# Optimization experiments

Measured on AMD Instinct MI355X. Metric: run time of the kernel, lower is better.

Reference implementation:

```python
import jax, jax.numpy as jnp
import numpy as np

DIM = 1024
NUM_HEADS = 16
HEAD_DIM = DIM // NUM_HEADS
PHI = (1 + 5 ** 0.5) / 2


def setup_inputs() -> dict:
    key = jax.random.key(0)
    ks = jax.random.split(key, 9)
    s = 1.0 / np.sqrt(DIM)
    x = jax.random.normal(ks[0], (1, 4096, DIM), dtype=jnp.float32)
    Wq = jax.random.uniform(ks[1], (DIM, DIM), jnp.float32, -s, s)
    bq = jax.random.uniform(ks[2], (DIM,), jnp.float32, -s, s)
    Wk = jax.random.uniform(ks[3], (DIM, DIM), jnp.float32, -s, s)
    bk = jax.random.uniform(ks[4], (DIM,), jnp.float32, -s, s)
    Wv = jax.random.uniform(ks[5], (DIM, DIM), jnp.float32, -s, s)
    bv = jax.random.uniform(ks[6], (DIM,), jnp.float32, -s, s)
    Wo = jax.random.uniform(ks[7], (DIM, DIM), jnp.float32, -s, s)
    bo = jax.random.uniform(ks[8], (DIM,), jnp.float32, -s, s)
    return {"x": x, "Wq": Wq, "bq": bq, "Wk": Wk, "bk": bk,
            "Wv": Wv, "bv": bv, "Wo": Wo, "bo": bo}


def reference(x, Wq, bq, Wk, bk, Wv, bv, Wo, bo):
    B, S, _ = x.shape
    H, D = NUM_HEADS, HEAD_DIM
    scale = D ** (-0.5)
    # projections, reshape to [B, H, S, D]
    q = (x @ Wq.T + bq).reshape(B, S, H, D).transpose(0, 2, 1, 3)
    k = (x @ Wk.T + bk).reshape(B, S, H, D).transpose(0, 2, 1, 3)
    v = (x @ Wv.T + bv).reshape(B, S, H, D).transpose(0, 2, 1, 3)
    attn = jnp.einsum('bhqd,bhkd->bhqk', q, k) * scale
    attn = jax.nn.softmax(attn, axis=-1)
    # fractal per-head scalar modulation: phi^{-i} for head i
    scales = PHI ** (-jnp.arange(H, dtype=jnp.float32))
    attn = attn * scales[None, :, None, None]
    out = jnp.einsum('bhqk,bhkd->bhqd', attn, v)
    out = out.transpose(0, 2, 1, 3).reshape(B, S, H * D)
    return out @ Wo.T + bo
```

## Files before the change

kernel.cpp:

```cpp
#include <hip/hip_runtime.h>


typedef unsigned short u16;
typedef unsigned int u32;
typedef __attribute__((ext_vector_type(8))) short short8;
typedef __attribute__((ext_vector_type(4))) float f32x4;
typedef __attribute__((ext_vector_type(4))) u16 u16x4;
typedef __attribute__((ext_vector_type(4))) u32 u32x4;

#define KDIM 1024
#define QSCALE 0.18033688011112042f
#define LOG2PHI 0.6942419136306174f

__device__ __forceinline__ u16 f2bf(float f) {
  u32 u = __builtin_bit_cast(u32, f);
  u32 r = (u + 0x7fffu + ((u >> 16) & 1u)) >> 16;
  return (u16)r;
}

__device__ __forceinline__ u32 cvtpk(float lo, float hi) {
  u32 r;
  asm("v_cvt_pk_bf16_f32 %0, %1, %2" : "=v"(r) : "v"(lo), "v"(hi));
  return r;
}

#define EXP2(x) __builtin_amdgcn_exp2f(x)

__device__ __forceinline__ f32x4 fzero() {
  f32x4 z; z[0] = 0.f; z[1] = 0.f; z[2] = 0.f; z[3] = 0.f; return z;
}

__global__ __launch_bounds__(256) void cvt_kernel(const float* __restrict__ src,
                                                  u16* __restrict__ dst, int n4) {
  int i = blockIdx.x * 256 + threadIdx.x;
  if (i >= n4) return;
  f32x4 v = *(const f32x4*)(src + (size_t)i * 4);
  u16x4 o;
  o[0] = f2bf(v[0]); o[1] = f2bf(v[1]); o[2] = f2bf(v[2]); o[3] = f2bf(v[3]);
  *(u16x4*)(dst + (size_t)i * 4) = o;
}

template <int MODE>
__global__ __launch_bounds__(256) void gemm_bt(
    const u16* __restrict__ A, const u16* __restrict__ Bw,
    const float* __restrict__ bias0, const float* __restrict__ bias1,
    const float* __restrict__ bias2,
    u16* __restrict__ qo, u16* __restrict__ ko, u16* __restrict__ vto,
    float* __restrict__ co) {
  __shared__ u16 As[128 * 64];
  __shared__ u16 Bs[128 * 64];
  const int tid = threadIdx.x;
  const int w = tid >> 6, lane = tid & 63;
  const int wr = w >> 1, wc = w & 1;
  const int bm = blockIdx.x, bn = blockIdx.y;
  const int lr = lane & 15, lg = lane >> 4;
  const int srow8 = lane >> 3;
  const int schunk = lane & 7;

  f32x4 acc[4][4];
#pragma unroll
  for (int m = 0; m < 4; ++m)
#pragma unroll
    for (int n = 0; n < 4; ++n) acc[m][n] = fzero();

  for (int kt = 0; kt < KDIM / 64; ++kt) {
#pragma unroll
    for (int it = 0; it < 4; ++it) {
      const int rowt = (w * 4 + it) * 8 + srow8;
      const int ck = schunk ^ (rowt & 7);
      const u16* sa = A + (size_t)(bm * 128 + rowt) * KDIM + kt * 64 + ck * 8;
      const u16* sb = Bw + (size_t)(bn * 128 + rowt) * KDIM + kt * 64 + ck * 8;
      auto ga = (const __attribute__((address_space(1))) u32*)sa;
      auto la = (__attribute__((address_space(3))) u32*)&As[(w * 4 + it) * 512];
      __builtin_amdgcn_global_load_lds(ga, la, 16, 0, 0);
      auto gb = (const __attribute__((address_space(1))) u32*)sb;
      auto lb = (__attribute__((address_space(3))) u32*)&Bs[(w * 4 + it) * 512];
      __builtin_amdgcn_global_load_lds(gb, lb, 16, 0, 0);
    }
    __syncthreads();
#pragma unroll
    for (int kk = 0; kk < 2; ++kk) {
      short8 af[4], bf[4];
#pragma unroll
      for (int m = 0; m < 4; ++m) {
        const int row = wr * 64 + m * 16 + lr;
        const int kb = kk * 64 + lg * 16;
        af[m] = *(const short8*)((const char*)As + row * 128 + (kb ^ ((row & 7) << 4)));
      }
#pragma unroll
      for (int n = 0; n < 4; ++n) {
        const int row = wc * 64 + n * 16 + lr;
        const int kb = kk * 64 + lg * 16;
        bf[n] = *(const short8*)((const char*)Bs + row * 128 + (kb ^ ((row & 7) << 4)));
      }
#pragma unroll
      for (int m = 0; m < 4; ++m)
#pragma unroll
        for (int n = 0; n < 4; ++n)
          acc[m][n] = __builtin_amdgcn_mfma_f32_16x16x32_bf16(af[m], bf[n], acc[m][n], 0, 0, 0);
    }
    __syncthreads();
  }

#pragma unroll
  for (int m = 0; m < 4; ++m) {
#pragma unroll
    for (int n = 0; n < 4; ++n) {
#pragma unroll
      for (int r = 0; r < 4; ++r) {
        const int srow = bm * 128 + wr * 64 + m * 16 + lg * 4 + r;
        const int col = bn * 128 + wc * 64 + n * 16 + lr;
        float v = acc[m][n][r];
        if (MODE == 0) {
          const int which = col >> 10;
          const int hd = col & 1023;
          const int h = hd >> 6, d = hd & 63;
          const float* bp = (which == 0) ? bias0 : (which == 1) ? bias1 : bias2;
          v += bp[hd];
          if (which == 0) {
            qo[(size_t)h * 262144 + (size_t)srow * 64 + d] = f2bf(v * QSCALE);
          } else if (which == 1) {
            ko[(size_t)h * 262144 + (size_t)srow * 64 + d] = f2bf(v);
          } else {
            const int k5 = srow & 31;
            const int kap = ((k5 >> 2) & 3) * 8 + ((k5 >> 4) & 1) * 4 + (k5 & 3);
            vto[(size_t)h * 262144 + (size_t)d * 4096 + (srow & ~31) + kap] = f2bf(v);
          }
        } else {
          co[(size_t)srow * 1024 + col] = v + bias0[col];
        }
      }
    }
  }
}

__global__ __launch_bounds__(256) void attn_kernel(const u16* __restrict__ Q,
                                                   const u16* __restrict__ K,
                                                   const u16* __restrict__ VT,
                                                   u16* __restrict__ O) {
  __shared__ u16 Ks[2][2][4096];
  __shared__ u16 Vs[2][2][4096];
  const int tid = threadIdx.x;
  const int w = tid >> 6, lane = tid & 63;
  const int qsub = w >> 1, kh = w & 1;
  const int bid = blockIdx.x;
  const int id2 = (bid & 7) * 64 + (bid >> 3);
  const int h = id2 >> 5, qt = id2 & 31;
  const int lr = lane & 15, lg = lane >> 4;
  const int qrow0 = qt * 128 + qsub * 64;

  const u16* kg = K + (size_t)h * 262144;
  const u16* vg = VT + (size_t)h * 262144;

  short8 qf[4][2];
#pragma unroll
  for (int qg = 0; qg < 4; ++qg)
#pragma unroll
    for (int dg = 0; dg < 2; ++dg)
      qf[qg][dg] = *(const short8*)(Q + (size_t)h * 262144 +
                                    (size_t)(qrow0 + qg * 16 + lr) * 64 + dg * 32 + lg * 8);

#define STAGE1(KH, B, J)                                                      \
  do {                                                                        \
    _Pragma("unroll")                                                         \
    for (int it = 0; it < 2; ++it) {                                          \
      const int c = it * 256 + tid;                                           \
      const int row = c >> 3;                                                 \
      const int sc = (c & 7) ^ (row & 7);                                     \
      const u16* gk = kg + (size_t)((J) + row) * 64 + sc * 8;                 \
      __builtin_amdgcn_global_load_lds(                                       \
          (const __attribute__((address_space(1))) u32*)gk,                   \
          (__attribute__((address_space(3))) u32*)&Ks[KH][B][c * 8], 16, 0, 0); \
      const u16* gv = vg + (size_t)row * 4096 + (J) + sc * 8;                 \
      __builtin_amdgcn_global_load_lds(                                       \
          (const __attribute__((address_space(1))) u32*)gv,                   \
          (__attribute__((address_space(3))) u32*)&Vs[KH][B][c * 8], 16, 0, 0); \
    }                                                                         \
  } while (0)
#define STAGE(B, T) do { STAGE1(0, B, (T) * 64); STAGE1(1, B, 2048 + (T) * 64); } while (0)

  f32x4 o[4][4];
#pragma unroll
  for (int dg = 0; dg < 4; ++dg)
#pragma unroll
    for (int qg = 0; qg < 4; ++qg) o[dg][qg] = fzero();
  float lsum[4] = {0.f, 0.f, 0.f, 0.f};

  STAGE(0, 0);
  __syncthreads();

  int b = 0;
  for (int t = 0; t < 32; ++t) {
    if (t < 31) STAGE(b ^ 1, t + 1);
    u32x4 pb[2][4];
#pragma unroll
    for (int half = 0; half < 2; ++half) {
      f32x4 s[2][4];
#pragma unroll
      for (int ki = 0; ki < 2; ++ki) {
        const int row = (half * 2 + ki) * 16 + lr;
        const int sw = (row & 7) << 4;
        const char* base = (const char*)&Ks[kh][b][0] + row * 128;
        const short8 k0 = *(const short8*)(base + ((lg * 16) ^ sw));
        const short8 k1 = *(const short8*)(base + ((64 + lg * 16) ^ sw));
#pragma unroll
        for (int qg = 0; qg < 4; ++qg) {
          s[ki][qg] = __builtin_amdgcn_mfma_f32_16x16x32_bf16(k0, qf[qg][0], fzero(), 0, 0, 0);
          s[ki][qg] = __builtin_amdgcn_mfma_f32_16x16x32_bf16(k1, qf[qg][1], s[ki][qg], 0, 0, 0);
        }
      }
#pragma unroll
      for (int qg = 0; qg < 4; ++qg) {
        float rs = 0.f;
#pragma unroll
        for (int ki = 0; ki < 2; ++ki)
#pragma unroll
          for (int r = 0; r < 4; ++r) {
            const float e = EXP2(s[ki][qg][r]);
            s[ki][qg][r] = e;
            rs += e;
          }
        lsum[qg] += rs;
        pb[half][qg][0] = cvtpk(s[0][qg][0], s[0][qg][1]);
        pb[half][qg][1] = cvtpk(s[0][qg][2], s[0][qg][3]);
        pb[half][qg][2] = cvtpk(s[1][qg][0], s[1][qg][1]);
        pb[half][qg][3] = cvtpk(s[1][qg][2], s[1][qg][3]);
      }
    }
#pragma unroll
    for (int dg = 0; dg < 4; ++dg) {
      const int row = dg * 16 + lr;
      const int sw = (row & 7) << 4;
      const char* base = (const char*)&Vs[kh][b][0] + row * 128;
      const short8 v0 = *(const short8*)(base + ((lg * 16) ^ sw));
      const short8 v1 = *(const short8*)(base + ((64 + lg * 16) ^ sw));
#pragma unroll
      for (int qg = 0; qg < 4; ++qg) {
        o[dg][qg] = __builtin_amdgcn_mfma_f32_16x16x32_bf16(
            v0, __builtin_bit_cast(short8, pb[0][qg]), o[dg][qg], 0, 0, 0);
        o[dg][qg] = __builtin_amdgcn_mfma_f32_16x16x32_bf16(
            v1, __builtin_bit_cast(short8, pb[1][qg]), o[dg][qg], 0, 0, 0);
      }
    }
    __syncthreads();
    b ^= 1;
  }
#undef STAGE
#undef STAGE1

#pragma unroll
  for (int qg = 0; qg < 4; ++qg) {
    lsum[qg] += __shfl_xor(lsum[qg], 16, 64);
    lsum[qg] += __shfl_xor(lsum[qg], 32, 64);
  }

  float* cO = (float*)&Ks[0][0][0];
  float* cL = (float*)&Vs[0][0][0];
  if (kh == 1) {
#pragma unroll
    for (int qg = 0; qg < 4; ++qg) {
#pragma unroll
      for (int dg = 0; dg < 4; ++dg)
        *(f32x4*)(cO + qsub * 4096 + (qg * 4 + dg) * 256 + lane * 4) = o[dg][qg];
      cL[qsub * 64 + qg * 16 + lr] = lsum[qg];
    }
  }
  __syncthreads();
  if (kh == 0) {
    const float hs = EXP2(-(float)h * LOG2PHI);
#pragma unroll
    for (int qg = 0; qg < 4; ++qg) {
      const float l = fmaxf(lsum[qg] + cL[qsub * 64 + qg * 16 + lr], 1e-10f);
      const float sc = hs / l;
#pragma unroll
      for (int dg = 0; dg < 4; ++dg) {
        const f32x4 oth = *(const f32x4*)(cO + qsub * 4096 + (qg * 4 + dg) * 256 + lane * 4);
        u16x4 pk;
#pragma unroll
        for (int r = 0; r < 4; ++r) pk[r] = f2bf((o[dg][qg][r] + oth[r]) * sc);
        *(u16x4*)(O + (size_t)(qrow0 + qg * 16 + lr) * 1024 + h * 64 + dg * 16 + lg * 4) = pk;
      }
    }
  }
}

extern "C" void kernel_launch(void* const* d_in, const int* in_sizes, int n_in,
                              void* d_out, int out_size, void* d_ws, size_t ws_size,
                              hipStream_t stream) {
  const float* x = (const float*)d_in[0];
  const float* Wq = (const float*)d_in[1];
  const float* bq = (const float*)d_in[2];
  const float* Wk = (const float*)d_in[3];
  const float* bk = (const float*)d_in[4];
  const float* Wv = (const float*)d_in[5];
  const float* bv = (const float*)d_in[6];
  const float* Wo = (const float*)d_in[7];
  const float* bo = (const float*)d_in[8];
  float* out = (float*)d_out;

  u16* xb = (u16*)d_ws;
  u16* wqkv = xb + 4194304;
  u16* wob = wqkv + 3145728;
  u16* qs = wob + 1048576;
  u16* ks = qs + 4194304;
  u16* vt = ks + 4194304;
  u16* ob = xb;

  cvt_kernel<<<4096, 256, 0, stream>>>(x, xb, 1048576);
  cvt_kernel<<<1024, 256, 0, stream>>>(Wq, wqkv, 262144);
  cvt_kernel<<<1024, 256, 0, stream>>>(Wk, wqkv + 1048576, 262144);
  cvt_kernel<<<1024, 256, 0, stream>>>(Wv, wqkv + 2097152, 262144);
  cvt_kernel<<<1024, 256, 0, stream>>>(Wo, wob, 262144);

  gemm_bt<0><<<dim3(32, 24), 256, 0, stream>>>(xb, wqkv, bq, bk, bv, qs, ks, vt, nullptr);
  attn_kernel<<<512, 256, 0, stream>>>(qs, ks, vt, ob);
  gemm_bt<1><<<dim3(32, 8), 256, 0, stream>>>(ob, wob, bo, nullptr, nullptr,
                                              nullptr, nullptr, nullptr, out);
}
```

Baseline: 168.0 us.

## Store V in MFMA fragment order and load it directly to registers

The QKV projection now writes V in a layout where each lane's 8-element MFMA operand is contiguous. This lets the attention kernel load V fragments straight from global memory into registers instead of staging them through LDS, which frees half the shared memory and removes the V LDS traffic. The five weight and input conversion launches are also merged into one kernel. The trade-off is that V loads are issued synchronously each iteration without double buffering, so their latency may be exposed.

```diff
diff --git a/kernel.cpp b/kernel.cpp
--- a/kernel.cpp
+++ b/kernel.cpp
@@ -30,14 +30,24 @@
   f32x4 z; z[0] = 0.f; z[1] = 0.f; z[2] = 0.f; z[3] = 0.f; return z;
 }
 
-__global__ __launch_bounds__(256) void cvt_kernel(const float* __restrict__ src,
-                                                  u16* __restrict__ dst, int n4) {
-  int i = blockIdx.x * 256 + threadIdx.x;
-  if (i >= n4) return;
-  f32x4 v = *(const f32x4*)(src + (size_t)i * 4);
+__global__ __launch_bounds__(256) void cvt_all(
+    const float* __restrict__ x, const float* __restrict__ wq,
+    const float* __restrict__ wk, const float* __restrict__ wv,
+    const float* __restrict__ wo, u16* __restrict__ xb,
+    u16* __restrict__ wqkv, u16* __restrict__ wob) {
+  const int i = blockIdx.x * 256 + threadIdx.x;
+  const float* src;
+  u16* dst;
+  int off;
+  if (i < 1048576) { src = x; dst = xb; off = i; }
+  else if (i < 1310720) { src = wq; dst = wqkv; off = i - 1048576; }
+  else if (i < 1572864) { src = wk; dst = wqkv + 1048576; off = i - 1310720; }
+  else if (i < 1835008) { src = wv; dst = wqkv + 2097152; off = i - 1572864; }
+  else { src = wo; dst = wob; off = i - 1835008; }
+  f32x4 v = *(const f32x4*)(src + (size_t)off * 4);
   u16x4 o;
   o[0] = f2bf(v[0]); o[1] = f2bf(v[1]); o[2] = f2bf(v[2]); o[3] = f2bf(v[3]);
-  *(u16x4*)(dst + (size_t)i * 4) = o;
+  *(u16x4*)(dst + (size_t)off * 4) = o;
 }
 
 template <int MODE>
@@ -122,9 +132,10 @@
           } else if (which == 1) {
             ko[(size_t)h * 262144 + (size_t)srow * 64 + d] = f2bf(v);
           } else {
-            const int k5 = srow & 31;
-            const int kap = ((k5 >> 2) & 3) * 8 + ((k5 >> 4) & 1) * 4 + (k5 & 3);
-            vto[(size_t)h * 262144 + (size_t)d * 4096 + (srow & ~31) + kap] = f2bf(v);
+            const int kb5 = ((srow >> 2) & 3) * 8 + ((srow >> 4) & 1) * 4 + (srow & 3);
+            const int lane2 = (kb5 >> 3) * 16 + (d & 15);
+            vto[((size_t)h * 128 + (srow >> 5)) * 2048 + (d >> 4) * 512 +
+                lane2 * 8 + (kb5 & 7)] = f2bf(v);
           }
         } else {
           co[(size_t)srow * 1024 + col] = v + bias0[col];
@@ -139,7 +150,7 @@
                                                    const u16* __restrict__ VT,
                                                    u16* __restrict__ O) {
   __shared__ u16 Ks[2][2][4096];
-  __shared__ u16 Vs[2][2][4096];
+  __shared__ float cL[128];
   const int tid = threadIdx.x;
   const int w = tid >> 6, lane = tid & 63;
   const int qsub = w >> 1, kh = w & 1;
@@ -171,10 +182,6 @@
       __builtin_amdgcn_global_load_lds(                                       \
           (const __attribute__((address_space(1))) u32*)gk,                   \
           (__attribute__((address_space(3))) u32*)&Ks[KH][B][c * 8], 16, 0, 0); \
-      const u16* gv = vg + (size_t)row * 4096 + (J) + sc * 8;                 \
-      __builtin_amdgcn_global_load_lds(                                       \
-          (const __attribute__((address_space(1))) u32*)gv,                   \
-          (__attribute__((address_space(3))) u32*)&Vs[KH][B][c * 8], 16, 0, 0); \
     }                                                                         \
   } while (0)
 #define STAGE(B, T) do { STAGE1(0, B, (T) * 64); STAGE1(1, B, 2048 + (T) * 64); } while (0)
@@ -192,6 +199,11 @@
   int b = 0;
   for (int t = 0; t < 32; ++t) {
     if (t < 31) STAGE(b ^ 1, t + 1);
+    const u16* vbase = vg + (size_t)(kh * 64 + t * 2) * 2048 + lane * 8;
+    short8 vf[8];
+#pragma unroll
+    for (int i = 0; i < 8; ++i) vf[i] = *(const short8*)(vbase + i * 512);
+
     u32x4 pb[2][4];
 #pragma unroll
     for (int half = 0; half < 2; ++half) {
@@ -229,17 +241,12 @@
     }
 #pragma unroll
     for (int dg = 0; dg < 4; ++dg) {
-      const int row = dg * 16 + lr;
-      const int sw = (row & 7) << 4;
-      const char* base = (const char*)&Vs[kh][b][0] + row * 128;
-      const short8 v0 = *(const short8*)(base + ((lg * 16) ^ sw));
-      const short8 v1 = *(const short8*)(base + ((64 + lg * 16) ^ sw));
 #pragma unroll
       for (int qg = 0; qg < 4; ++qg) {
         o[dg][qg] = __builtin_amdgcn_mfma_f32_16x16x32_bf16(
-            v0, __builtin_bit_cast(short8, pb[0][qg]), o[dg][qg], 0, 0, 0);
+            vf[dg], __builtin_bit_cast(short8, pb[0][qg]), o[dg][qg], 0, 0, 0);
         o[dg][qg] = __builtin_amdgcn_mfma_f32_16x16x32_bf16(
-            v1, __builtin_bit_cast(short8, pb[1][qg]), o[dg][qg], 0, 0, 0);
+            vf[4 + dg], __builtin_bit_cast(short8, pb[1][qg]), o[dg][qg], 0, 0, 0);
       }
     }
     __syncthreads();
@@ -255,7 +262,6 @@
   }
 
   float* cO = (float*)&Ks[0][0][0];
-  float* cL = (float*)&Vs[0][0][0];
   if (kh == 1) {
 #pragma unroll
     for (int qg = 0; qg < 4; ++qg) {
@@ -306,11 +312,7 @@
   u16* vt = ks + 4194304;
   u16* ob = xb;
 
-  cvt_kernel<<<4096, 256, 0, stream>>>(x, xb, 1048576);
-  cvt_kernel<<<1024, 256, 0, stream>>>(Wq, wqkv, 262144);
-  cvt_kernel<<<1024, 256, 0, stream>>>(Wk, wqkv + 1048576, 262144);
-  cvt_kernel<<<1024, 256, 0, stream>>>(Wv, wqkv + 2097152, 262144);
-  cvt_kernel<<<1024, 256, 0, stream>>>(Wo, wob, 262144);
+  cvt_all<<<8192, 256, 0, stream>>>(x, Wq, Wk, Wv, Wo, xb, wqkv, wob);
 
   gemm_bt<0><<<dim3(32, 24), 256, 0, stream>>>(xb, wqkv, bq, bk, bv, qs, ks, vt, nullptr);
   attn_kernel<<<512, 256, 0, stream>>>(qs, ks, vt, ob);
```

Result: slower. 184.3 us (+9.7%).
